# Optimization experiments

Hardware: AMD Instinct MI355X
Metric: run time of the kernel (lower is better)

## Reference

```python
import jax, jax.numpy as jnp
import numpy as np

NU, NI, DU, DI, E, B, T = 100000, 50000, 256, 256, 128, 8192, 24

def setup_inputs() -> dict:
    key = jax.random.key(0)
    ks = jax.random.split(key, 12)
    s = 0.05
    return {
        "nodes": jax.random.randint(ks[0], (B,), 0, NU),
        "neigh_idx": jax.random.randint(ks[1], (B, T), 0, NI),
        "u_weight": jax.random.normal(ks[2], (NU, DU), jnp.float32),
        "i_weight": jax.random.normal(ks[3], (NI, DI), jnp.float32),
        "uW": jax.random.normal(ks[4], (DU, E), jnp.float32) * s,
        "ub": jnp.zeros((E,), jnp.float32),
        "iW": jax.random.normal(ks[5], (DI, E), jnp.float32) * s,
        "ib": jnp.zeros((E,), jnp.float32),
        "aW1": jax.random.normal(ks[6], (2 * E, E), jnp.float32) * s,
        "ab1": jnp.zeros((E,), jnp.float32),
        "aW2": jax.random.normal(ks[7], (E, E), jnp.float32) * s,
        "ab2": jnp.zeros((E,), jnp.float32),
        "aW3": jax.random.normal(ks[8], (E, 1), jnp.float32) * s,
        "ab3": jnp.zeros((1,), jnp.float32),
    }


def reference(nodes, neigh_idx, u_weight, i_weight, uW, ub, iW, ib,
              aW1, ab1, aW2, ab2, aW3, ab3):
    # node features: u_layer(ufeature.weight[nodes])  -> [B, E]
    nodes_fea = u_weight[nodes] @ uW + ub
    # neighbor features: i_layer(ifeature.weight[interactions]) -> [B, T, E]
    neighs = i_weight[neigh_idx] @ iW + ib
    # attention MLP over cat(neigh_feat, node_feat.repeat) -> softmax over T
    x = jnp.concatenate(
        [neighs, jnp.broadcast_to(nodes_fea[:, None, :], neighs.shape)], axis=-1)
    h = jax.nn.relu(x @ aW1 + ab1)
    h = jax.nn.relu(h @ aW2 + ab2)
    logits = (h @ aW3 + ab3)[..., 0]            # [B, T]
    att = jax.nn.softmax(logits, axis=-1)       # softmax over neighbors (dim=0 per node)
    # attention-weighted aggregation: neighs_feature.T @ att_w  -> [B, E]
    agg = jnp.einsum('bt,bte->be', att, neighs)
    # scatter into embed_matrix rows of the batch nodes
    embed_matrix = jnp.zeros((NU, E), jnp.float32).at[nodes].set(agg)
    return nodes_fea, embed_matrix
```

## Files before the change

kernel.cpp:

```cpp
#include <hip/hip_runtime.h>
#include <math.h>

#define NU 100000
#define NI 50000
#define DK 256
#define EN 128
#define BB 8192
#define TT 24

typedef short short8 __attribute__((ext_vector_type(8)));
typedef float f32x4  __attribute__((ext_vector_type(4)));

#define WPACK_SHORTS 114688
#define WP_OFF     0
#define OWNER_OFF  229376
#define NTAB_OFF   629376
#define NPART_OFF  13429376

#define OFF_IWT   0
#define OFF_UWT   32768
#define OFF_AW1UT 65536
#define OFF_AW1LT 81920
#define OFF_AW2T  98304

#define NBLK_NEIGH 782
#define NBLK_NF    128
#define NBLK_PACK  448
#define GGA 4
#define ATTN_BLKS  (BB / GGA)

__device__ __forceinline__ unsigned short f2b(float x) {
    unsigned int u = __float_as_uint(x);
    u = (u + 0x7FFFu + ((u >> 16) & 1u)) >> 16;
    return (unsigned short)u;
}
__device__ __forceinline__ float b2f(unsigned short v) {
    return __uint_as_float(((unsigned int)v) << 16);
}
__device__ __forceinline__ unsigned int cvtpk_bf16(float lo, float hi) {
    unsigned int r;
    asm("v_cvt_pk_bf16_f32 %0, %1, %2" : "=v"(r) : "v"(lo), "v"(hi));
    return r;
}

#define MFMA(a, b, c) __builtin_amdgcn_mfma_f32_16x16x32_bf16((a), (b), (c), 0, 0, 0)
#define LDROW(buf, stride, row, k) \
    (*reinterpret_cast<const short8*>(reinterpret_cast<const char*>(buf) + (row) * (stride) + (k) * 2))

__global__ __launch_bounds__(256)
void prep_kernel(const int* __restrict__ nodes,
                 const float* __restrict__ uW, const float* __restrict__ iW,
                 const float* __restrict__ aW1, const float* __restrict__ aW2,
                 short* __restrict__ wp, int* __restrict__ owner)
{
    if (blockIdx.x < NBLK_PACK) {
        int i = blockIdx.x * 256 + threadIdx.x;
        float v;
        if (i < 32768)      { int j = i;         int n = j >> 8, k = j & 255; v = iW[k * EN + n]; }
        else if (i < 65536) { int j = i - 32768; int n = j >> 8, k = j & 255; v = uW[k * EN + n]; }
        else if (i < 81920) { int j = i - 65536; int n = j >> 7, k = j & 127; v = aW1[k * EN + n]; }
        else if (i < 98304) { int j = i - 81920; int n = j >> 7, k = j & 127; v = aW1[(128 + k) * EN + n]; }
        else                { int j = i - 98304; int n = j >> 7, k = j & 127; v = aW2[k * EN + n]; }
        wp[i] = (short)f2b(v);
    } else {
        int b = (blockIdx.x - NBLK_PACK) * 256 + threadIdx.x;
        if (b < BB) owner[nodes[b]] = -1;
    }
}

__global__ __launch_bounds__(256, 4)
void embed_kernel(const int* __restrict__ nodes,
                  const float* __restrict__ u_weight, const float* __restrict__ i_weight,
                  const float* __restrict__ ub, const float* __restrict__ ib,
                  const float* __restrict__ ab1,
                  const short* __restrict__ wp, int* __restrict__ owner,
                  short* __restrict__ ntab, float* __restrict__ out_nf,
                  float* __restrict__ npart, float* __restrict__ out_embed)
{
    __shared__ __align__(16) char smem[33792];
    __shared__ int sNd[64];

    const int tid = threadIdx.x;
    const int l = tid & 63, lr = l & 15, lq = l >> 4, n0 = (tid >> 6) * 32;
    const int kA = lq * 8, nc0 = n0 + lr, nc1 = n0 + 16 + lr;

    if (blockIdx.x < NBLK_NEIGH) {
        const int r0 = blockIdx.x * 64;
        const int nrows = (NI - r0 < 64) ? (NI - r0) : 64;

        for (int task = tid; task < 64 * 32; task += 256) {
            int row = task >> 5, c = task & 31;
            if (row < nrows) {
                const float* src = i_weight + (size_t)(r0 + row) * DK + c * 8;
                float4 f0 = *(const float4*)src;
                float4 f1 = *(const float4*)(src + 4);
                short8 o;
                o[0]=f2b(f0.x); o[1]=f2b(f0.y); o[2]=f2b(f0.z); o[3]=f2b(f0.w);
                o[4]=f2b(f1.x); o[5]=f2b(f1.y); o[6]=f2b(f1.z); o[7]=f2b(f1.w);
                *reinterpret_cast<short8*>(smem + row * 528 + c * 16) = o;
            }
        }
        __syncthreads();

        const short* iWt = wp + OFF_IWT;
        f32x4 acc[4][2];
        #pragma unroll
        for (int m = 0; m < 4; ++m) { acc[m][0] = {0.f,0.f,0.f,0.f}; acc[m][1] = {0.f,0.f,0.f,0.f}; }
        #pragma unroll
        for (int ks = 0; ks < 8; ++ks) {
            int k = ks * 32 + kA;
            short8 w0 = *reinterpret_cast<const short8*>(iWt + nc0 * DK + k);
            short8 w1 = *reinterpret_cast<const short8*>(iWt + nc1 * DK + k);
            #pragma unroll
            for (int m = 0; m < 4; ++m) {
                short8 a = LDROW(smem, 528, m * 16 + lr, k);
                acc[m][0] = MFMA(a, w0, acc[m][0]);
                acc[m][1] = MFMA(a, w1, acc[m][1]);
            }
        }
        __syncthreads();
        {
            float ib0 = ib[nc0], ib1 = ib[nc1];
            #pragma unroll
            for (int m = 0; m < 4; ++m)
                #pragma unroll
                for (int nt = 0; nt < 2; ++nt) {
                    int n = nt ? nc1 : nc0;
                    float bv = nt ? ib1 : ib0;
                    #pragma unroll
                    for (int r = 0; r < 4; ++r) {
                        int row = m * 16 + lq * 4 + r;
                        *reinterpret_cast<short*>(smem + row * 264 + n * 2)
                            = (short)f2b(acc[m][nt][r] + bv);
                    }
                }
        }
        __syncthreads();
        for (int g = tid; g < nrows * 16; g += 256) {
            int row = g >> 4, s = g & 15;
            short8 v = *reinterpret_cast<const short8*>(smem + row * 264 + s * 16);
            *reinterpret_cast<short8*>(ntab + (size_t)(r0 + row) * EN + s * 8) = v;
        }
    } else {
        const int bblk = blockIdx.x - NBLK_NEIGH;
        const int r0 = bblk * 64;
        {
            int bq = bblk * 256 + tid;
            if (bq < BB) atomicMax(&owner[nodes[bq]], bq);
        }
        if (tid < 64) sNd[tid] = nodes[r0 + tid];
        __syncthreads();

        for (int task = tid; task < 64 * 32; task += 256) {
            int row = task >> 5, c = task & 31;
            const float* src = u_weight + (size_t)sNd[row] * DK + c * 8;
            float4 f0 = *(const float4*)src;
            float4 f1 = *(const float4*)(src + 4);
            short8 o;
            o[0]=f2b(f0.x); o[1]=f2b(f0.y); o[2]=f2b(f0.z); o[3]=f2b(f0.w);
            o[4]=f2b(f1.x); o[5]=f2b(f1.y); o[6]=f2b(f1.z); o[7]=f2b(f1.w);
            *reinterpret_cast<short8*>(smem + row * 528 + c * 16) = o;
        }
        __syncthreads();

        const short* uWt   = wp + OFF_UWT;
        const short* aW1Lt = wp + OFF_AW1LT;

        f32x4 acc[4][2];
        #pragma unroll
        for (int m = 0; m < 4; ++m) { acc[m][0] = {0.f,0.f,0.f,0.f}; acc[m][1] = {0.f,0.f,0.f,0.f}; }
        #pragma unroll
        for (int ks = 0; ks < 8; ++ks) {
            int k = ks * 32 + kA;
            short8 w0 = *reinterpret_cast<const short8*>(uWt + nc0 * DK + k);
            short8 w1 = *reinterpret_cast<const short8*>(uWt + nc1 * DK + k);
            #pragma unroll
            for (int m = 0; m < 4; ++m) {
                short8 a = LDROW(smem, 528, m * 16 + lr, k);
                acc[m][0] = MFMA(a, w0, acc[m][0]);
                acc[m][1] = MFMA(a, w1, acc[m][1]);
            }
        }
        __syncthreads();
        {
            float b0v = ub[nc0], b1v = ub[nc1];
            #pragma unroll
            for (int m = 0; m < 4; ++m)
                #pragma unroll
                for (int nt = 0; nt < 2; ++nt) {
                    int n = nt ? nc1 : nc0;
                    float bv = nt ? b1v : b0v;
                    #pragma unroll
                    for (int r = 0; r < 4; ++r) {
                        int row = m * 16 + lq * 4 + r;
                        float v = acc[m][nt][r] + bv;
                        out_nf[(size_t)(r0 + row) * EN + n] = v;
                        *reinterpret_cast<short*>(smem + row * 272 + n * 2) = (short)f2b(v);
                    }
                }
        }
        __syncthreads();

        f32x4 ap[4][2];
        #pragma unroll
        for (int m = 0; m < 4; ++m) { ap[m][0] = {0.f,0.f,0.f,0.f}; ap[m][1] = {0.f,0.f,0.f,0.f}; }
        #pragma unroll
        for (int ks = 0; ks < 4; ++ks) {
            int k = ks * 32 + kA;
            short8 w0 = *reinterpret_cast<const short8*>(aW1Lt + nc0 * EN + k);
            short8 w1 = *reinterpret_cast<const short8*>(aW1Lt + nc1 * EN + k);
            #pragma unroll
            for (int m = 0; m < 4; ++m) {
                short8 a = LDROW(smem, 272, m * 16 + lr, k);
                ap[m][0] = MFMA(a, w0, ap[m][0]);
                ap[m][1] = MFMA(a, w1, ap[m][1]);
            }
        }
        {
            float b0v = ab1[nc0], b1v = ab1[nc1];
            #pragma unroll
            for (int m = 0; m < 4; ++m)
                #pragma unroll
                for (int nt = 0; nt < 2; ++nt) {
                    int n = nt ? nc1 : nc0;
                    float bv = nt ? b1v : b0v;
                    #pragma unroll
                    for (int r = 0; r < 4; ++r) {
                        int row = m * 16 + lq * 4 + r;
                        npart[(size_t)(r0 + row) * EN + n] = ap[m][nt][r] + bv;
                    }
                }
        }
    }

    {
        float4* embed4 = (float4*)out_embed;
        const int n16 = NU * EN / 4;
        const int gsz = (NBLK_NEIGH + NBLK_NF) * 256;
        float4 z = {0.f, 0.f, 0.f, 0.f};
        for (int i = blockIdx.x * 256 + tid; i < n16; i += gsz) embed4[i] = z;
    }
}

__global__ __launch_bounds__(256, 2)
void attn_kernel(const int* __restrict__ nodes, const int* __restrict__ neigh_idx,
                 const float* __restrict__ ab2, const float* __restrict__ aW3,
                 const float* __restrict__ ab3, const short* __restrict__ wp,
                 const short* __restrict__ ntab, const float* __restrict__ npart,
                 const int* __restrict__ owner, float* __restrict__ out_embed)
{
    __shared__ __align__(16) short sNg[96 * 136];
    __shared__ __align__(16) short sH1[96 * 136];
    __shared__ float sNpF[512];
    __shared__ float sLogP[4][96];

    const int tid = threadIdx.x;
    const int b0  = blockIdx.x * GGA;
    const int l   = tid & 63, w = tid >> 6;
    const int lr  = l & 15, lq = l >> 4;
    const int n0  = w * 32;
    const int kA  = lq * 8, nc0 = n0 + lr, nc1 = n0 + 16 + lr;

    sNpF[tid]       = npart[(size_t)b0 * EN + tid];
    sNpF[tid + 256] = npart[(size_t)b0 * EN + 256 + tid];

    #pragma unroll
    for (int j = 0; j < 6; ++j) {
        int task = j * 64 + l;
        int trow = task >> 4, s = task & 15;
        int idx = neigh_idx[(b0 + w) * TT + trow];
        short8 v = *reinterpret_cast<const short8*>(ntab + (size_t)idx * EN + s * 8);
        *reinterpret_cast<short8*>(reinterpret_cast<char*>(sNg) + (w * 24 + trow) * 272 + s * 16) = v;
    }
    __syncthreads();

    const short* aW1Ut = wp + OFF_AW1UT;
    const short* aW2t  = wp + OFF_AW2T;

    f32x4 acc[6][2];
    #pragma unroll
    for (int m = 0; m < 6; ++m) { acc[m][0] = {0.f,0.f,0.f,0.f}; acc[m][1] = {0.f,0.f,0.f,0.f}; }
    #pragma unroll
    for (int ks = 0; ks < 4; ++ks) {
        int k = ks * 32 + kA;
        short8 w0 = *reinterpret_cast<const short8*>(aW1Ut + nc0 * EN + k);
        short8 w1 = *reinterpret_cast<const short8*>(aW1Ut + nc1 * EN + k);
        #pragma unroll
        for (int m = 0; m < 6; ++m) {
            short8 a = LDROW(sNg, 272, m * 16 + lr, k);
            acc[m][0] = MFMA(a, w0, acc[m][0]);
            acc[m][1] = MFMA(a, w1, acc[m][1]);
        }
    }
    #pragma unroll
    for (int m = 0; m < 6; ++m) {
        int g = (m == 0) ? 0 : (m == 1) ? ((lq < 2) ? 0 : 1)
              : (m == 2) ? 1 : (m == 3) ? 2 : (m == 4) ? ((lq < 2) ? 2 : 3) : 3;
        #pragma unroll
        for (int nt = 0; nt < 2; ++nt) {
            int n = nt ? nc1 : nc0;
            float np = sNpF[g * EN + n];
            float v0 = fmaxf(acc[m][nt][0] + np, 0.f);
            float v1 = fmaxf(acc[m][nt][1] + np, 0.f);
            float v2 = fmaxf(acc[m][nt][2] + np, 0.f);
            float v3 = fmaxf(acc[m][nt][3] + np, 0.f);
            unsigned int p01 = cvtpk_bf16(v0, v1);
            unsigned int p23 = cvtpk_bf16(v2, v3);
            char* base = reinterpret_cast<char*>(sH1) + (m * 16 + lq * 4) * 272 + n * 2;
            *reinterpret_cast<short*>(base)       = (short)(p01 & 0xFFFF);
            *reinterpret_cast<short*>(base + 272) = (short)(p01 >> 16);
            *reinterpret_cast<short*>(base + 544) = (short)(p23 & 0xFFFF);
            *reinterpret_cast<short*>(base + 816) = (short)(p23 >> 16);
        }
    }
    __syncthreads();

    #pragma unroll
    for (int m = 0; m < 6; ++m) { acc[m][0] = {0.f,0.f,0.f,0.f}; acc[m][1] = {0.f,0.f,0.f,0.f}; }
    #pragma unroll
    for (int ks = 0; ks < 4; ++ks) {
        int k = ks * 32 + kA;
        short8 w0 = *reinterpret_cast<const short8*>(aW2t + nc0 * EN + k);
        short8 w1 = *reinterpret_cast<const short8*>(aW2t + nc1 * EN + k);
        #pragma unroll
        for (int m = 0; m < 6; ++m) {
            short8 a = LDROW(sH1, 272, m * 16 + lr, k);
            acc[m][0] = MFMA(a, w0, acc[m][0]);
            acc[m][1] = MFMA(a, w1, acc[m][1]);
        }
    }
    {
        float b0v = ab2[nc0], b1v = ab2[nc1];
        float w3a = aW3[nc0], w3b = aW3[nc1];
        #pragma unroll
        for (int m = 0; m < 6; ++m) {
            float lp[4];
            #pragma unroll
            for (int r = 0; r < 4; ++r) {
                float v0 = fmaxf(acc[m][0][r] + b0v, 0.f);
                float v1 = fmaxf(acc[m][1][r] + b1v, 0.f);
                lp[r] = v0 * w3a + v1 * w3b;
            }
            #pragma unroll
            for (int r = 0; r < 4; ++r) {
                float v = lp[r];
                v += __shfl_xor(v, 1, 16);
                v += __shfl_xor(v, 2, 16);
                v += __shfl_xor(v, 4, 16);
                v += __shfl_xor(v, 8, 16);
                if (lr == 0) sLogP[w][m * 16 + lq * 4 + r] = v;
            }
        }
    }
    __syncthreads();

    float lg = -1e30f;
    if (l < TT)
        lg = sLogP[0][w * 24 + l] + sLogP[1][w * 24 + l]
           + sLogP[2][w * 24 + l] + sLogP[3][w * 24 + l] + ab3[0];
    float mx = lg;
    #pragma unroll
    for (int d = 32; d > 0; d >>= 1) mx = fmaxf(mx, __shfl_xor(mx, d, 64));
    float p = (l < TT) ? __expf(lg - mx) : 0.f;
    float s = p;
    #pragma unroll
    for (int d = 32; d > 0; d >>= 1) s += __shfl_xor(s, d, 64);
    float att = p / s;

    {
        float a0 = 0.f, a1 = 0.f;
        #pragma unroll
        for (int t = 0; t < TT; ++t) {
            float wt = __shfl(att, t, 64);
            const char* rbase = reinterpret_cast<const char*>(sNg) + (w * 24 + t) * 272;
            a0 += wt * b2f(*reinterpret_cast<const unsigned short*>(rbase + l * 2));
            a1 += wt * b2f(*reinterpret_cast<const unsigned short*>(rbase + (l + 64) * 2));
        }
        int node = nodes[b0 + w];
        if (owner[node] == b0 + w) {
            out_embed[(size_t)node * EN + l]      = a0;
            out_embed[(size_t)node * EN + 64 + l] = a1;
        }
    }
}

extern "C" void kernel_launch(void* const* d_in, const int* in_sizes, int n_in,
                              void* d_out, int out_size, void* d_ws, size_t ws_size,
                              hipStream_t stream) {
    const int*   nodes     = (const int*)d_in[0];
    const int*   neigh_idx = (const int*)d_in[1];
    const float* u_weight  = (const float*)d_in[2];
    const float* i_weight  = (const float*)d_in[3];
    const float* uW  = (const float*)d_in[4];
    const float* ub  = (const float*)d_in[5];
    const float* iW  = (const float*)d_in[6];
    const float* ib  = (const float*)d_in[7];
    const float* aW1 = (const float*)d_in[8];
    const float* ab1 = (const float*)d_in[9];
    const float* aW2 = (const float*)d_in[10];
    const float* ab2 = (const float*)d_in[11];
    const float* aW3 = (const float*)d_in[12];
    const float* ab3 = (const float*)d_in[13];

    float* out_nf    = (float*)d_out;
    float* out_embed = out_nf + (size_t)BB * EN;

    char*  ws    = (char*)d_ws;
    short* wpack = (short*)(ws + WP_OFF);
    int*   owner = (int*)(ws + OWNER_OFF);
    short* ntab  = (short*)(ws + NTAB_OFF);
    float* npart = (float*)(ws + NPART_OFF);

    prep_kernel<<<NBLK_PACK + 32, 256, 0, stream>>>(nodes, uW, iW, aW1, aW2, wpack, owner);
    embed_kernel<<<NBLK_NEIGH + NBLK_NF, 256, 0, stream>>>(
        nodes, u_weight, i_weight, ub, ib, ab1, wpack, owner, ntab, out_nf, npart, out_embed);
    attn_kernel<<<ATTN_BLKS, 256, 0, stream>>>(nodes, neigh_idx, ab2, aW3, ab3,
                                               wpack, ntab, npart, owner, out_embed);
}
```

Baseline: 79.78 us.

## Precompute per-item first attention layer and register-resident attention MLP

Computes the neighbor half of the first attention layer once per item row in the embedding kernel and stores it as a bf16 table. The attention kernel gathers these precomputed rows, adds the node partial and relu, and feeds them straight into the second-layer MFMA per wave, removing the first GEMM and shared H1 staging and block syncs. This trades redundant per-pair matmul work for an extra table write and gather plus an additional bf16 rounding step.

```diff
diff --git a/kernel.cpp b/kernel.cpp
--- a/kernel.cpp
+++ b/kernel.cpp
@@ -16,6 +16,7 @@
 #define OWNER_OFF  229376
 #define NTAB_OFF   629376
 #define NPART_OFF  13429376
+#define ATAB_OFF   17623680
 
 #define OFF_IWT   0
 #define OFF_UWT   32768
@@ -41,6 +42,15 @@
     unsigned int r;
     asm("v_cvt_pk_bf16_f32 %0, %1, %2" : "=v"(r) : "v"(lo), "v"(hi));
     return r;
+}
+__device__ __forceinline__ short8 pack8(float v0, float v1, float v2, float v3,
+                                        float v4, float v5, float v6, float v7) {
+    union { short8 s; unsigned int u[4]; } x;
+    x.u[0] = cvtpk_bf16(v0, v1);
+    x.u[1] = cvtpk_bf16(v2, v3);
+    x.u[2] = cvtpk_bf16(v4, v5);
+    x.u[3] = cvtpk_bf16(v6, v7);
+    return x.s;
 }
 
 #define MFMA(a, b, c) __builtin_amdgcn_mfma_f32_16x16x32_bf16((a), (b), (c), 0, 0, 0)
@@ -74,8 +84,9 @@
                   const float* __restrict__ ub, const float* __restrict__ ib,
                   const float* __restrict__ ab1,
                   const short* __restrict__ wp, int* __restrict__ owner,
-                  short* __restrict__ ntab, float* __restrict__ out_nf,
-                  float* __restrict__ npart, float* __restrict__ out_embed)
+                  short* __restrict__ ntab, short* __restrict__ atab,
+                  float* __restrict__ out_nf, float* __restrict__ npart,
+                  float* __restrict__ out_embed)
 {
     __shared__ __align__(16) char smem[33792];
     __shared__ int sNd[64];
@@ -136,10 +147,48 @@
                 }
         }
         __syncthreads();
+
         for (int g = tid; g < nrows * 16; g += 256) {
             int row = g >> 4, s = g & 15;
             short8 v = *reinterpret_cast<const short8*>(smem + row * 264 + s * 16);
             *reinterpret_cast<short8*>(ntab + (size_t)(r0 + row) * EN + s * 8) = v;
+        }
+        const short* aW1Ut = wp + OFF_AW1UT;
+        f32x4 ac2[4][2];
+        #pragma unroll
+        for (int m = 0; m < 4; ++m) { ac2[m][0] = {0.f,0.f,0.f,0.f}; ac2[m][1] = {0.f,0.f,0.f,0.f}; }
+        #pragma unroll
+        for (int ks = 0; ks < 4; ++ks) {
+            int k = ks * 32 + kA;
+            short8 w0 = *reinterpret_cast<const short8*>(aW1Ut + nc0 * EN + k);
+            short8 w1 = *reinterpret_cast<const short8*>(aW1Ut + nc1 * EN + k);
+            #pragma unroll
+            for (int m = 0; m < 4; ++m) {
+                short8 a = LDROW(smem, 264, m * 16 + lr, k);
+                ac2[m][0] = MFMA(a, w0, ac2[m][0]);
+                ac2[m][1] = MFMA(a, w1, ac2[m][1]);
+            }
+        }
+        {
+            char* up = smem + 16896;
+            #pragma unroll
+            for (int m = 0; m < 4; ++m)
+                #pragma unroll
+                for (int nt = 0; nt < 2; ++nt) {
+                    int n = nt ? nc1 : nc0;
+                    #pragma unroll
+                    for (int r = 0; r < 4; ++r) {
+                        int row = m * 16 + lq * 4 + r;
+                        *reinterpret_cast<short*>(up + row * 264 + n * 2)
+                            = (short)f2b(ac2[m][nt][r]);
+                    }
+                }
+        }
+        __syncthreads();
+        for (int g = tid; g < nrows * 16; g += 256) {
+            int row = g >> 4, s = g & 15;
+            short8 v = *reinterpret_cast<const short8*>(smem + 16896 + row * 264 + s * 16);
+            *reinterpret_cast<short8*>(atab + (size_t)(r0 + row) * EN + s * 8) = v;
         }
     } else {
         const int bblk = blockIdx.x - NBLK_NEIGH;
@@ -242,122 +291,95 @@
     }
 }
 
-__global__ __launch_bounds__(256, 2)
+__global__ __launch_bounds__(256)
 void attn_kernel(const int* __restrict__ nodes, const int* __restrict__ neigh_idx,
                  const float* __restrict__ ab2, const float* __restrict__ aW3,
-                 const float* __restrict__ ab3, const short* __restrict__ wp,
-                 const short* __restrict__ ntab, const float* __restrict__ npart,
+                 const short* __restrict__ wp, const short* __restrict__ ntab,
+                 const short* __restrict__ atab, const float* __restrict__ npart,
                  const int* __restrict__ owner, float* __restrict__ out_embed)
 {
-    __shared__ __align__(16) short sNg[96 * 136];
-    __shared__ __align__(16) short sH1[96 * 136];
-    __shared__ float sNpF[512];
-    __shared__ float sLogP[4][96];
+    __shared__ __align__(16) short sNg[GGA][24 * 136];
+    __shared__ float sLg[GGA][32];
 
     const int tid = threadIdx.x;
-    const int b0  = blockIdx.x * GGA;
-    const int l   = tid & 63, w = tid >> 6;
-    const int lr  = l & 15, lq = l >> 4;
-    const int n0  = w * 32;
-    const int kA  = lq * 8, nc0 = n0 + lr, nc1 = n0 + 16 + lr;
-
-    sNpF[tid]       = npart[(size_t)b0 * EN + tid];
-    sNpF[tid + 256] = npart[(size_t)b0 * EN + 256 + tid];
+    const int w = tid >> 6, l = tid & 63;
+    const int lr = l & 15, lq = l >> 4;
+    const int b = blockIdx.x * GGA + w;
+    const int ibase = b * TT;
 
     #pragma unroll
     for (int j = 0; j < 6; ++j) {
         int task = j * 64 + l;
         int trow = task >> 4, s = task & 15;
-        int idx = neigh_idx[(b0 + w) * TT + trow];
+        int idx = neigh_idx[ibase + trow];
         short8 v = *reinterpret_cast<const short8*>(ntab + (size_t)idx * EN + s * 8);
-        *reinterpret_cast<short8*>(reinterpret_cast<char*>(sNg) + (w * 24 + trow) * 272 + s * 16) = v;
-    }
-    __syncthreads();
-
-    const short* aW1Ut = wp + OFF_AW1UT;
-    const short* aW2t  = wp + OFF_AW2T;
-
-    f32x4 acc[6][2];
-    #pragma unroll
-    for (int m = 0; m < 6; ++m) { acc[m][0] = {0.f,0.f,0.f,0.f}; acc[m][1] = {0.f,0.f,0.f,0.f}; }
+        *reinterpret_cast<short8*>(reinterpret_cast<char*>(&sNg[w][0]) + trow * 272 + s * 16) = v;
+    }
+
+    const int rowA1 = (16 + lr < TT) ? (16 + lr) : 0;
+    const int idxA0 = neigh_idx[ibase + lr];
+    const int idxA1 = neigh_idx[ibase + rowA1];
+
+    short8 afr0[4], afr1[4];
     #pragma unroll
     for (int ks = 0; ks < 4; ++ks) {
-        int k = ks * 32 + kA;
-        short8 w0 = *reinterpret_cast<const short8*>(aW1Ut + nc0 * EN + k);
-        short8 w1 = *reinterpret_cast<const short8*>(aW1Ut + nc1 * EN + k);
-        #pragma unroll
-        for (int m = 0; m < 6; ++m) {
-            short8 a = LDROW(sNg, 272, m * 16 + lr, k);
-            acc[m][0] = MFMA(a, w0, acc[m][0]);
-            acc[m][1] = MFMA(a, w1, acc[m][1]);
-        }
-    }
-    #pragma unroll
-    for (int m = 0; m < 6; ++m) {
-        int g = (m == 0) ? 0 : (m == 1) ? ((lq < 2) ? 0 : 1)
-              : (m == 2) ? 1 : (m == 3) ? 2 : (m == 4) ? ((lq < 2) ? 2 : 3) : 3;
-        #pragma unroll
-        for (int nt = 0; nt < 2; ++nt) {
-            int n = nt ? nc1 : nc0;
-            float np = sNpF[g * EN + n];
-            float v0 = fmaxf(acc[m][nt][0] + np, 0.f);
-            float v1 = fmaxf(acc[m][nt][1] + np, 0.f);
-            float v2 = fmaxf(acc[m][nt][2] + np, 0.f);
-            float v3 = fmaxf(acc[m][nt][3] + np, 0.f);
-            unsigned int p01 = cvtpk_bf16(v0, v1);
-            unsigned int p23 = cvtpk_bf16(v2, v3);
-            char* base = reinterpret_cast<char*>(sH1) + (m * 16 + lq * 4) * 272 + n * 2;
-            *reinterpret_cast<short*>(base)       = (short)(p01 & 0xFFFF);
-            *reinterpret_cast<short*>(base + 272) = (short)(p01 >> 16);
-            *reinterpret_cast<short*>(base + 544) = (short)(p23 & 0xFFFF);
-            *reinterpret_cast<short*>(base + 816) = (short)(p23 >> 16);
-        }
-    }
-    __syncthreads();
-
-    #pragma unroll
-    for (int m = 0; m < 6; ++m) { acc[m][0] = {0.f,0.f,0.f,0.f}; acc[m][1] = {0.f,0.f,0.f,0.f}; }
-    #pragma unroll
-    for (int ks = 0; ks < 4; ++ks) {
-        int k = ks * 32 + kA;
-        short8 w0 = *reinterpret_cast<const short8*>(aW2t + nc0 * EN + k);
-        short8 w1 = *reinterpret_cast<const short8*>(aW2t + nc1 * EN + k);
-        #pragma unroll
-        for (int m = 0; m < 6; ++m) {
-            short8 a = LDROW(sH1, 272, m * 16 + lr, k);
-            acc[m][0] = MFMA(a, w0, acc[m][0]);
-            acc[m][1] = MFMA(a, w1, acc[m][1]);
-        }
-    }
-    {
-        float b0v = ab2[nc0], b1v = ab2[nc1];
-        float w3a = aW3[nc0], w3b = aW3[nc1];
-        #pragma unroll
-        for (int m = 0; m < 6; ++m) {
-            float lp[4];
-            #pragma unroll
-            for (int r = 0; r < 4; ++r) {
-                float v0 = fmaxf(acc[m][0][r] + b0v, 0.f);
-                float v1 = fmaxf(acc[m][1][r] + b1v, 0.f);
-                lp[r] = v0 * w3a + v1 * w3b;
-            }
-            #pragma unroll
-            for (int r = 0; r < 4; ++r) {
-                float v = lp[r];
-                v += __shfl_xor(v, 1, 16);
-                v += __shfl_xor(v, 2, 16);
-                v += __shfl_xor(v, 4, 16);
-                v += __shfl_xor(v, 8, 16);
-                if (lr == 0) sLogP[w][m * 16 + lq * 4 + r] = v;
-            }
-        }
-    }
-    __syncthreads();
-
-    float lg = -1e30f;
-    if (l < TT)
-        lg = sLogP[0][w * 24 + l] + sLogP[1][w * 24 + l]
-           + sLogP[2][w * 24 + l] + sLogP[3][w * 24 + l] + ab3[0];
+        int e0 = ks * 32 + lq * 8;
+        float4 np0 = *reinterpret_cast<const float4*>(npart + (size_t)b * EN + e0);
+        float4 np1 = *reinterpret_cast<const float4*>(npart + (size_t)b * EN + e0 + 4);
+        short8 a0 = *reinterpret_cast<const short8*>(atab + (size_t)idxA0 * EN + e0);
+        short8 a1 = *reinterpret_cast<const short8*>(atab + (size_t)idxA1 * EN + e0);
+        afr0[ks] = pack8(
+            fmaxf(b2f((unsigned short)a0[0]) + np0.x, 0.f), fmaxf(b2f((unsigned short)a0[1]) + np0.y, 0.f),
+            fmaxf(b2f((unsigned short)a0[2]) + np0.z, 0.f), fmaxf(b2f((unsigned short)a0[3]) + np0.w, 0.f),
+            fmaxf(b2f((unsigned short)a0[4]) + np1.x, 0.f), fmaxf(b2f((unsigned short)a0[5]) + np1.y, 0.f),
+            fmaxf(b2f((unsigned short)a0[6]) + np1.z, 0.f), fmaxf(b2f((unsigned short)a0[7]) + np1.w, 0.f));
+        afr1[ks] = pack8(
+            fmaxf(b2f((unsigned short)a1[0]) + np0.x, 0.f), fmaxf(b2f((unsigned short)a1[1]) + np0.y, 0.f),
+            fmaxf(b2f((unsigned short)a1[2]) + np0.z, 0.f), fmaxf(b2f((unsigned short)a1[3]) + np0.w, 0.f),
+            fmaxf(b2f((unsigned short)a1[4]) + np1.x, 0.f), fmaxf(b2f((unsigned short)a1[5]) + np1.y, 0.f),
+            fmaxf(b2f((unsigned short)a1[6]) + np1.z, 0.f), fmaxf(b2f((unsigned short)a1[7]) + np1.w, 0.f));
+    }
+
+    const short* aW2t = wp + OFF_AW2T;
+    f32x4 acc0[8], acc1[8];
+    #pragma unroll
+    for (int nt = 0; nt < 8; ++nt) { acc0[nt] = {0.f,0.f,0.f,0.f}; acc1[nt] = {0.f,0.f,0.f,0.f}; }
+    #pragma unroll
+    for (int nt = 0; nt < 8; ++nt) {
+        int nrow = nt * 16 + lr;
+        #pragma unroll
+        for (int ks = 0; ks < 4; ++ks) {
+            short8 wv = *reinterpret_cast<const short8*>(aW2t + nrow * EN + ks * 32 + lq * 8);
+            acc0[nt] = MFMA(afr0[ks], wv, acc0[nt]);
+            acc1[nt] = MFMA(afr1[ks], wv, acc1[nt]);
+        }
+    }
+
+    float lp0[4] = {0.f,0.f,0.f,0.f}, lp1[4] = {0.f,0.f,0.f,0.f};
+    #pragma unroll
+    for (int nt = 0; nt < 8; ++nt) {
+        int c = nt * 16 + lr;
+        float bv = ab2[c], wv = aW3[c];
+        #pragma unroll
+        for (int r = 0; r < 4; ++r) {
+            lp0[r] += fmaxf(acc0[nt][r] + bv, 0.f) * wv;
+            lp1[r] += fmaxf(acc1[nt][r] + bv, 0.f) * wv;
+        }
+    }
+    #pragma unroll
+    for (int r = 0; r < 4; ++r) {
+        float v0 = lp0[r], v1 = lp1[r];
+        v0 += __shfl_xor(v0, 1, 16); v0 += __shfl_xor(v0, 2, 16);
+        v0 += __shfl_xor(v0, 4, 16); v0 += __shfl_xor(v0, 8, 16);
+        v1 += __shfl_xor(v1, 1, 16); v1 += __shfl_xor(v1, 2, 16);
+        v1 += __shfl_xor(v1, 4, 16); v1 += __shfl_xor(v1, 8, 16);
+        if (lr == 0) {
+            sLg[w][lq * 4 + r]      = v0;
+            sLg[w][16 + lq * 4 + r] = v1;
+        }
+    }
+
+    float lg = (l < TT) ? sLg[w][l] : -1e30f;
     float mx = lg;
     #pragma unroll
     for (int d = 32; d > 0; d >>= 1) mx = fmaxf(mx, __shfl_xor(mx, d, 64));
@@ -372,12 +394,12 @@
         #pragma unroll
         for (int t = 0; t < TT; ++t) {
             float wt = __shfl(att, t, 64);
-            const char* rbase = reinterpret_cast<const char*>(sNg) + (w * 24 + t) * 272;
+            const char* rbase = reinterpret_cast<const char*>(&sNg[w][0]) + t * 272;
             a0 += wt * b2f(*reinterpret_cast<const unsigned short*>(rbase + l * 2));
             a1 += wt * b2f(*reinterpret_cast<const unsigned short*>(rbase + (l + 64) * 2));
         }
-        int node = nodes[b0 + w];
-        if (owner[node] == b0 + w) {
+        int node = nodes[b];
+        if (owner[node] == b) {
             out_embed[(size_t)node * EN + l]      = a0;
             out_embed[(size_t)node * EN + 64 + l] = a1;
         }
@@ -400,7 +422,6 @@
     const float* aW2 = (const float*)d_in[10];
     const float* ab2 = (const float*)d_in[11];
     const float* aW3 = (const float*)d_in[12];
-    const float* ab3 = (const float*)d_in[13];
 
     float* out_nf    = (float*)d_out;
     float* out_embed = out_nf + (size_t)BB * EN;
@@ -410,10 +431,11 @@
     int*   owner = (int*)(ws + OWNER_OFF);
     short* ntab  = (short*)(ws + NTAB_OFF);
     float* npart = (float*)(ws + NPART_OFF);
+    short* atab  = (short*)(ws + ATAB_OFF);
 
     prep_kernel<<<NBLK_PACK + 32, 256, 0, stream>>>(nodes, uW, iW, aW1, aW2, wpack, owner);
     embed_kernel<<<NBLK_NEIGH + NBLK_NF, 256, 0, stream>>>(
-        nodes, u_weight, i_weight, ub, ib, ab1, wpack, owner, ntab, out_nf, npart, out_embed);
-    attn_kernel<<<ATTN_BLKS, 256, 0, stream>>>(nodes, neigh_idx, ab2, aW3, ab3,
-                                               wpack, ntab, npart, owner, out_embed);
-}
+        nodes, u_weight, i_weight, ub, ib, ab1, wpack, owner, ntab, atab, out_nf, npart, out_embed);
+    attn_kernel<<<ATTN_BLKS, 256, 0, stream>>>(nodes, neigh_idx, ab2, aW3,
+                                               wpack, ntab, atab, npart, owner, out_embed);
+}
```

After: 92.53 us. 1.16x slower.
